# Kernel tuning notes

Hardware: AMD Instinct MI355X
Metric: run time of the kernel (lower is better)

## Reference

```python
import jax, jax.numpy as jnp
import numpy as np

# ---- production-scale dims ----
U, I, D = 51200, 25600, 64          # users, items, embed_size
E, EP = 1_000_000, 100_000          # train edges, pos/neg scoring edges
K = 8                               # topk similar users (FFT filter length)
NF = K // 2 + 1                     # rfft bins
CL_BS = 256                         # contrastive chunk size (U % CL_BS == 0)
TEMP = 0.2                          # args.temperature
N_LAYERS = 2                        # args.layers


def setup_inputs() -> dict:
    key = jax.random.key(0)
    ks = jax.random.split(key, 14)
    return {
        "user_emb": jax.random.normal(ks[0], (U, D), jnp.float32) * 0.1,
        "item_emb": jax.random.normal(ks[1], (I, D), jnp.float32) * 0.1,
        "W": jax.random.normal(ks[2], (D, D), jnp.float32) * (1.0 / np.sqrt(D)),
        "a": jax.random.normal(ks[3], (D,), jnp.float32) * 0.1,
        "WU": jax.random.normal(ks[4], (D, D), jnp.float32) * (1.0 / np.sqrt(D)),
        "aU": jax.random.normal(ks[5], (2 * D,), jnp.float32) * 0.1,
        "complex_weight": jax.random.normal(ks[6], (1, NF, D, 2), jnp.float32) * 0.02,
        "rate_src": jax.random.randint(ks[7], (E,), 0, U),
        "rate_dst": jax.random.randint(ks[8], (E,), 0, I),
        "pos_u": jax.random.randint(ks[9], (EP,), 0, U),
        "pos_i": jax.random.randint(ks[10], (EP,), 0, I),
        "neg_u": jax.random.randint(ks[11], (EP,), 0, U),
        "neg_i": jax.random.randint(ks[12], (EP,), 0, I),
        "nbr_idx": jax.random.randint(ks[13], (U, K), 0, U),
    }


def _propagate(src_feat, src_idx, dst_idx, n_dst):
    """DGRecLayer: degree-normalized mean aggregation over bipartite edges."""
    msg = src_feat[src_idx]                                       # [E, D] gather
    agg = jax.ops.segment_sum(msg, dst_idx, num_segments=n_dst)   # [n_dst, D] scatter
    deg = jax.ops.segment_sum(jnp.ones((src_idx.shape[0],), src_feat.dtype),
                              dst_idx, num_segments=n_dst)
    return agg / jnp.maximum(deg, 1.0)[:, None]


def _layer_attention(ls, W, a):
    t = jnp.stack(ls, axis=0)                                     # [L+1, N, D]
    alpha = jax.nn.softmax(jnp.einsum('lnd,de,e->ln', t, W, a), axis=0)
    return jnp.einsum('lnd,ln->nd', t, alpha)


def _anchor_user_embed(user_emb, WU, aU, complex_weight, nbr_idx):
    # Original detaches user embeddings to numpy for the FAISS path.
    ue = jax.lax.stop_gradient(user_emb)
    simu = ue[nbr_idx]                                            # [U, K, D]
    x = jnp.fft.rfft(simu, axis=1, norm='ortho')                  # [U, NF, D]
    wc = complex_weight[..., 0] + 1j * complex_weight[..., 1]     # [1, NF, D]
    simu = jnp.fft.irfft(x * wc, n=K, axis=1, norm='ortho')       # [U, K, D]
    Wsimu = jnp.einsum('ukd,de->uke', simu, WU)                   # [U, K, D]
    Wu = jnp.broadcast_to((ue @ WU)[:, None, :], Wsimu.shape)     # [U, K, D]
    e = jnp.concatenate([Wsimu, Wu], axis=2) @ aU                 # [U, K]
    e = jnp.where(e > 0, e, 0.1 * e)                              # LeakyReLU(0.1)
    alpha = jax.nn.softmax(e, axis=1)
    return jnp.einsum('uke,uk->ue', Wsimu, alpha)                 # [U, D]


def _chunk_contrast(r1, r2):
    B = r1.shape[0]
    n1 = jnp.linalg.norm(r1, axis=-1, keepdims=True)
    n2 = jnp.linalg.norm(r2, axis=-1, keepdims=True)
    s11 = (r1 @ r1.T) / (n1 @ n1.T + 1e-6) / TEMP
    c12 = (r1 @ r2.T) / (n1 @ n2.T + 1e-6) / TEMP
    s22 = (r2 @ r2.T) / (n2 @ n2.T + 1e-6) / TEMP
    c21 = (r2 @ r1.T) / (n2 @ n1.T + 1e-6) / TEMP
    mask = jax.nn.one_hot(jnp.arange(B), 2 * B, dtype=r1.dtype) * (-1e10)
    logits = jnp.concatenate(
        [jnp.concatenate([s11, c12], axis=-1) + mask,
         jnp.concatenate([s22, c21], axis=-1) + mask], axis=0)     # [2B, 2B]
    labels = jnp.concatenate([jnp.arange(B) + B, jnp.arange(B) + B])
    logz = jax.scipy.special.logsumexp(logits, axis=-1)
    return logz - logits[jnp.arange(2 * B), labels]                # per-example CE


def reference(user_emb, item_emb, W, a, WU, aU, complex_weight,
              rate_src, rate_dst, pos_u, pos_i, neg_u, neg_i, nbr_idx):
    h_u, h_i = user_emb, item_emb
    users, items = [h_u], [h_i]
    for _ in range(N_LAYERS):
        new_i = _propagate(h_u, rate_src, rate_dst, I)   # user -> item ('rate')
        new_u = _propagate(h_i, rate_dst, rate_src, U)   # item -> user ('rated by')
        h_u, h_i = new_u, new_i
        users.append(h_u)
        items.append(h_i)
    hu = _layer_attention(users, W, a)                   # [U, D]
    hi = _layer_attention(items, W, a)                   # [I, D]

    anchor = _anchor_user_embed(user_emb, WU, aU, complex_weight, nbr_idx)
    r1 = hu.reshape(-1, CL_BS, D)
    r2 = anchor.reshape(-1, CL_BS, D)
    loss_contrast = jax.vmap(_chunk_contrast)(r1, r2).mean()

    score_pos = jnp.sum(hu[pos_u] * hi[pos_i], axis=-1, keepdims=True)  # u_dot_v
    score_neg = jnp.sum(hu[neg_u] * hi[neg_i], axis=-1, keepdims=True)
    return score_pos, score_neg, loss_contrast
```

## Files before the change

kernel.cpp:

```cpp
#include <hip/hip_runtime.h>
#include <hip/hip_bf16.h>

constexpr int U_  = 51200;
constexpr int I_  = 25600;
constexpr int E_  = 1000000;
constexpr int EP_ = 100000;
constexpr int CB_ = 256;
constexpr int NCHUNK_ = U_ / CB_;
constexpr size_t UD_ = (size_t)U_ * 64;
constexpr size_t ID_ = (size_t)I_ * 64;
constexpr int NBK_ = 200;
constexpr int CAP_ = 8192;
constexpr int TILE_ = 4096;
constexpr int NBA_ = (E_ + TILE_ - 1) / TILE_;
constexpr int NANC_ = U_ / 16;
constexpr int NCVT_ = (int)((UD_ + ID_) / 512);

constexpr float SCALE_E_  = 16.f;
constexpr float ISCALE_E_ = 1.f / 16.f;
constexpr float SCALE_1_  = 64.f;
constexpr float ISCALE_1_ = 1.f / 64.f;

constexpr size_t OFF_LOSS  = 0;
constexpr size_t OFF_FLAG  = 1;
constexpr size_t OFF_CURU  = 8;
constexpr size_t OFF_CURI  = 208;
constexpr size_t MEMSET_BYTES = 408 * 4;
constexpr size_t OFF_VEC   = 448;
constexpr size_t OFF_BBU   = 640;
constexpr size_t OFF_BBI   = 848;
constexpr size_t OFF_ROWU  = 1088;
constexpr size_t OFF_ROWI  = ((OFF_ROWU + U_ + 1 + 63) / 64) * 64;
constexpr size_t OFF_CSRU  = ((OFF_ROWI + I_ + 1 + 63) / 64) * 64;
constexpr size_t OFF_CSRI  = OFF_CSRU + E_;
constexpr size_t OFF_U1    = ((OFF_CSRI + E_ + 63) / 64) * 64;
constexpr size_t OFF_I1    = OFF_U1 + UD_;
constexpr size_t OFF_HU    = OFF_I1 + ID_;
constexpr size_t OFF_HI    = OFF_HU + UD_;
constexpr size_t OFF_ANC   = OFF_HI + ID_;
constexpr size_t OFF_UE8   = OFF_ANC + UD_;
constexpr size_t OFF_IE8   = OFF_UE8 + UD_ / 4;
constexpr size_t OFF_U18   = OFF_IE8 + ID_ / 4;
constexpr size_t OFF_I18   = OFF_U18 + UD_ / 4;

#define DEVI static __device__ __forceinline__

typedef _Float16 h2v __attribute__((ext_vector_type(2)));
typedef _Float16 f16x8 __attribute__((ext_vector_type(8)));
typedef float floatx4 __attribute__((ext_vector_type(4)));

DEVI float b2f(__hip_bfloat16 x) { return __bfloat162float(x); }

DEVI float ldf(const void* p, size_t i, int isf32) {
  if (isf32) return ((const float*)p)[i];
  return b2f(((const __hip_bfloat16*)p)[i]);
}

DEVI float frcp(float x) { return __builtin_amdgcn_rcpf(x); }

DEVI float fexp2(float x) {
#if __has_builtin(__builtin_amdgcn_exp2f)
  return __builtin_amdgcn_exp2f(x);
#else
  return exp2f(x);
#endif
}

DEVI float fp8_dec(unsigned v) {
#if __has_builtin(__builtin_amdgcn_cvt_f32_fp8)
  return __builtin_amdgcn_cvt_f32_fp8(v, 0);
#else
  unsigned b = v & 0xFF;
  if (!(b & 0x78)) return 0.f;
  unsigned short h = (unsigned short)(((b & 0x80) << 8) | (((b & 0x7f) + (8 << 3)) << 7));
  _Float16 hf; __builtin_memcpy(&hf, &h, 2);
  return (float)hf;
#endif
}
DEVI unsigned fp8_enc_pk(float a, float b) {
#if __has_builtin(__builtin_amdgcn_cvt_pk_fp8_f32)
  return __builtin_amdgcn_cvt_pk_fp8_f32(a, b, 0u, false);
#else
  auto enc1 = [](float f) -> unsigned {
    _Float16 hf = (_Float16)f; unsigned short hb; __builtin_memcpy(&hb, &hf, 2);
    int s = hb >> 15, e = (hb >> 10) & 31, m = hb & 1023;
    int e8 = e - 15 + 7;
    int m3 = (m + ((1 << 6) + ((m >> 7) & 1))) >> 7;
    if (m3 > 7) { m3 = 0; e8++; }
    if (e8 <= 0) return (unsigned)(s << 7);
    if (e8 > 15) { e8 = 15; m3 = 6; }
    return (unsigned)((s << 7) | (e8 << 3) | m3);
  };
  return enc1(a) | (enc1(b) << 8);
#endif
}

DEVI int waveInclScan(int v, int lane) {
  #pragma unroll
  for (int off = 1; off < 64; off <<= 1) {
    int t = __shfl_up(v, off, 64);
    if (lane >= off) v += t;
  }
  return v;
}

__global__ void prep_kernel(const unsigned short* __restrict__ ueu,
                            const void* __restrict__ W, const void* __restrict__ a,
                            const void* __restrict__ WU, const void* __restrict__ aU,
                            float* __restrict__ vecs, float* __restrict__ flag) {
  int cnt = 0;
  for (int i = 0; i < 256; i++) {
    int e = (ueu[i] >> 7) & 0xFF;
    if (e >= 130) cnt++;
  }
  int isf32 = (cnt >= 8);
  if (threadIdx.x == 0) *flag = isf32 ? 1.0f : 0.0f;
  int d = threadIdx.x;
  float s = 0.f, t1 = 0.f, t2 = 0.f;
  for (int e = 0; e < 64; e++) {
    s += ldf(W, d * 64 + e, isf32) * ldf(a, e, isf32);
    float wue = ldf(WU, d * 64 + e, isf32);
    t1 += wue * ldf(aU, e, isf32);
    t2 += wue * ldf(aU, 64 + e, isf32);
  }
  vecs[d] = s;
  vecs[64 + d] = t1;
  vecs[128 + d] = t2;
}

struct BktSmem {
  int histU[NBK_], histI[NBK_];
  int loffU[NBK_ + 1], loffI[NBK_ + 1];
  int cbU[NBK_], cbI[NBK_];
  int lcU[NBK_], lcI[NBK_];
  int wsU[4], wsI[4];
  unsigned recsU[TILE_], recsI[TILE_];
};
constexpr int WS_ = 72;
struct AncSmem {
  _Float16 WUt[64 * WS_];
  _Float16 mixS[16 * WS_];
  float invSe[16];
  int nbrS[128];
};
constexpr size_t FSA_SMEM = sizeof(BktSmem) > sizeof(AncSmem) ? sizeof(BktSmem) : sizeof(AncSmem);

DEVI void bucketA_body(char* smemRaw, int blk,
    const int* __restrict__ rs, const int* __restrict__ rd,
    unsigned* __restrict__ bufU, unsigned* __restrict__ bufI,
    int* __restrict__ curU, int* __restrict__ curI) {
  BktSmem& S = *(BktSmem*)smemRaw;
  int tid = threadIdx.x;
  int base = blk * TILE_;
  for (int i = tid; i < NBK_; i += 256) { S.histU[i] = 0; S.histI[i] = 0; }
  __syncthreads();
  int ss[16], dd[16];
  #pragma unroll
  for (int t = 0; t < 16; t++) {
    int e = base + t * 256 + tid;
    bool v = e < E_;
    ss[t] = v ? rs[e] : -1;
    dd[t] = v ? rd[e] : 0;
    if (v) {
      atomicAdd(&S.histU[ss[t] >> 8], 1);
      atomicAdd(&S.histI[dd[t] >> 7], 1);
    }
  }
  __syncthreads();
  if (tid < NBK_) {
    int cU = S.histU[tid];
    S.cbU[tid] = tid * CAP_ + (cU ? atomicAdd(&curU[tid], cU) : 0);
    int cI = S.histI[tid];
    S.cbI[tid] = tid * CAP_ + (cI ? atomicAdd(&curI[tid], cI) : 0);
  }
  int lane = tid & 63, wv = tid >> 6;
  int cvU = (tid < NBK_) ? S.histU[tid] : 0;
  int cvI = (tid < NBK_) ? S.histI[tid] : 0;
  int inU = waveInclScan(cvU, lane);
  int inI = waveInclScan(cvI, lane);
  if (lane == 63) { S.wsU[wv] = inU; S.wsI[wv] = inI; }
  __syncthreads();
  int woU = 0, woI = 0;
  for (int w = 0; w < wv; w++) { woU += S.wsU[w]; woI += S.wsI[w]; }
  if (tid < NBK_) {
    S.loffU[tid] = woU + inU - cvU;
    S.loffI[tid] = woI + inI - cvI;
  }
  if (tid == NBK_ - 1) {
    S.loffU[NBK_] = woU + inU;
    S.loffI[NBK_] = woI + inI;
  }
  __syncthreads();
  if (tid < NBK_) { S.lcU[tid] = S.loffU[tid]; S.lcI[tid] = S.loffI[tid]; }
  __syncthreads();
  #pragma unroll
  for (int t = 0; t < 16; t++) {
    if (ss[t] >= 0) {
      int b = ss[t] >> 8;
      int p = atomicAdd(&S.lcU[b], 1);
      S.recsU[p] = ((unsigned)(ss[t] & 255) << 17) | (unsigned)dd[t];
      b = dd[t] >> 7;
      p = atomicAdd(&S.lcI[b], 1);
      S.recsI[p] = ((unsigned)(dd[t] & 127) << 17) | (unsigned)ss[t];
    }
  }
  __syncthreads();
  int totU = S.loffU[NBK_];
  for (int p = tid; p < totU; p += 256) {
    int lo = 0, hi = NBK_;
    while (hi - lo > 1) { int mid = (lo + hi) >> 1; if (S.loffU[mid] <= p) lo = mid; else hi = mid; }
    bufU[S.cbU[lo] + (p - S.loffU[lo])] = S.recsU[p];
  }
  int totI = S.loffI[NBK_];
  for (int p = tid; p < totI; p += 256) {
    int lo = 0, hi = NBK_;
    while (hi - lo > 1) { int mid = (lo + hi) >> 1; if (S.loffI[mid] <= p) lo = mid; else hi = mid; }
    bufI[S.cbI[lo] + (p - S.loffI[lo])] = S.recsI[p];
  }
}

DEVI void anchor_body(char* smemRaw, int blk,
    const void* __restrict__ ue, const void* __restrict__ WU,
    const void* __restrict__ cw, const float* __restrict__ vecs,
    const int* __restrict__ nbr, float* __restrict__ out, int isf32) {
  AncSmem& S = *(AncSmem*)smemRaw;
  int tid = threadIdx.x;
  int wv = tid >> 6, lane = tid & 63;
  int ublk = blk * 16;

  #pragma unroll
  for (int it = 0; it < 16; it++) {
    int k = it * 4 + wv;
    S.WUt[lane * WS_ + k] = (_Float16)ldf(WU, (size_t)k * 64 + lane, isf32);
  }
  if (tid < 128) S.nbrS[tid] = nbr[ublk * 8 + tid];
  __syncthreads();

  float cw0 = ldf(cw, (0 * 64 + lane) * 2, isf32);
  float w1r = ldf(cw, (1 * 64 + lane) * 2, isf32), w1i = ldf(cw, (1 * 64 + lane) * 2 + 1, isf32);
  float w2r = ldf(cw, (2 * 64 + lane) * 2, isf32), w2i = ldf(cw, (2 * 64 + lane) * 2 + 1, isf32);
  float w3r = ldf(cw, (3 * 64 + lane) * 2, isf32), w3i = ldf(cw, (3 * 64 + lane) * 2 + 1, isf32);
  float cw4 = ldf(cw, (4 * 64 + lane) * 2, isf32);
  float v1 = vecs[64 + lane], v2 = vecs[128 + lane];
  const float c1 = 0.70710678118654752440f;

  float xc[8], xn[8];
  #pragma unroll
  for (int k = 0; k < 8; k++)
    xc[k] = ldf(ue, (size_t)S.nbrS[wv * 32 + k] * 64 + lane, isf32);

  for (int u4 = 0; u4 < 4; u4++) {
    int uL = wv * 4 + u4;
    int u = ublk + uL;
    if (u4 < 3) {
      #pragma unroll
      for (int k = 0; k < 8; k++)
        xn[k] = ldf(ue, (size_t)S.nbrS[wv * 32 + (u4 + 1) * 8 + k] * 64 + lane, isf32);
    }
    float sA = xc[1] - xc[3] - xc[5] + xc[7];
    float sB = xc[1] + xc[3] - xc[5] - xc[7];
    float ev = (xc[0] + xc[4]) + (xc[2] + xc[6]);
    float od = (xc[1] + xc[5]) + (xc[3] + xc[7]);
    float d04 = xc[0] - xc[4], d26 = xc[2] - xc[6];
    float X0r = ev + od;
    float X1r = d04 + c1 * sA;
    float X1i = -d26 - c1 * sB;
    float X2r = (xc[0] + xc[4]) - (xc[2] + xc[6]);
    float X2i = -(xc[1] - xc[3] + xc[5] - xc[7]);
    float X3r = d04 - c1 * sA;
    float X3i = d26 - c1 * sB;
    float X4r = ev - od;
    float Zr0 = X0r * cw0;
    float Zr1 = X1r * w1r - X1i * w1i, Zi1 = X1r * w1i + X1i * w1r;
    float Zr2 = X2r * w2r - X2i * w2i, Zi2 = X2r * w2i + X2i * w2r;
    float Zr3 = X3r * w3r - X3i * w3i, Zi3 = X3r * w3i + X3i * w3r;
    float Zr4 = X4r * cw4;
    float eP = Zr0 + Zr4, eM = Zr0 - Zr4;
    float t1 = c1 * (Zr1 - Zr3), t2 = c1 * (Zi1 + Zi3);
    float y[8];
    y[0] = eP + 2.f * (Zr1 + Zr2 + Zr3);
    y[1] = eM + 2.f * (t1 - t2 - Zi2);
    y[2] = eP + 2.f * (-Zi1 - Zr2 + Zi3);
    y[3] = eM + 2.f * (-t1 - t2 + Zi2);
    y[4] = eP + 2.f * (-Zr1 + Zr2 - Zr3);
    y[5] = eM + 2.f * (-t1 + t2 - Zi2);
    y[6] = eP + 2.f * (Zi1 - Zr2 - Zi3);
    y[7] = eM + 2.f * (t1 + t2 + Zi2);
    #pragma unroll
    for (int k = 0; k < 8; k++) y[k] *= 0.125f;

    float ek[8];
    #pragma unroll
    for (int k = 0; k < 8; k++) ek[k] = y[k] * v1;
    float q = ldf(ue, (size_t)u * 64 + lane, isf32) * v2;
    #pragma unroll
    for (int off = 32; off; off >>= 1) {
      #pragma unroll
      for (int k = 0; k < 8; k++) ek[k] += __shfl_xor(ek[k], off, 64);
      q += __shfl_xor(q, off, 64);
    }
    float m = -1e30f;
    #pragma unroll
    for (int k = 0; k < 8; k++) {
      float v = ek[k] + q;
      v = v > 0.f ? v : 0.1f * v;
      ek[k] = v;
      m = fmaxf(m, v);
    }
    float se = 0.f, wexp[8];
    #pragma unroll
    for (int k = 0; k < 8; k++) { wexp[k] = __expf(ek[k] - m); se += wexp[k]; }
    float mix = 0.f;
    #pragma unroll
    for (int k = 0; k < 8; k++) mix += wexp[k] * y[k];
    S.mixS[uL * WS_ + lane] = (_Float16)mix;
    if (lane == 0) S.invSe[uL] = frcp(se);
    #pragma unroll
    for (int k = 0; k < 8; k++) xc[k] = xn[k];
  }
  __syncthreads();

  int n = lane & 15, qd = lane >> 4;
  f16x8 A0 = *(const f16x8*)&S.mixS[(lane & 15) * WS_ + qd * 8];
  f16x8 A1 = *(const f16x8*)&S.mixS[(lane & 15) * WS_ + 32 + qd * 8];
  f16x8 B0 = *(const f16x8*)&S.WUt[(wv * 16 + n) * WS_ + qd * 8];
  f16x8 B1 = *(const f16x8*)&S.WUt[(wv * 16 + n) * WS_ + 32 + qd * 8];
  const floatx4 zero = {0.f, 0.f, 0.f, 0.f};
  floatx4 acc = __builtin_amdgcn_mfma_f32_16x16x32_f16(A0, B0, zero, 0, 0, 0);
  acc = __builtin_amdgcn_mfma_f32_16x16x32_f16(A1, B1, acc, 0, 0, 0);
  #pragma unroll
  for (int r = 0; r < 4; r++) {
    int m = qd * 4 + r;
    out[(size_t)(ublk + m) * 64 + wv * 16 + n] = acc[r] * S.invSe[m];
  }
}

DEVI void convert_body(int blk, const void* __restrict__ ue, const void* __restrict__ ie,
                       unsigned char* __restrict__ ue8, unsigned char* __restrict__ ie8,
                       int isf32) {
  size_t t = (size_t)blk * 256 + threadIdx.x;
  float a, b; unsigned short* dst; size_t o;
  if (t < UD_ / 2) {
    a = ldf(ue, 2 * t, isf32); b = ldf(ue, 2 * t + 1, isf32);
    dst = (unsigned short*)ue8; o = t;
  } else {
    size_t s = t - UD_ / 2;
    a = ldf(ie, 2 * s, isf32); b = ldf(ie, 2 * s + 1, isf32);
    dst = (unsigned short*)ie8; o = s;
  }
  unsigned p = fp8_enc_pk(a * SCALE_E_, b * SCALE_E_);
  dst[o] = (unsigned short)(p & 0xFFFF);
}

__global__ __launch_bounds__(256) void fusedA_kernel(
    const int* __restrict__ rs, const int* __restrict__ rd,
    unsigned* __restrict__ bufU, unsigned* __restrict__ bufI,
    int* __restrict__ curU, int* __restrict__ curI,
    const void* __restrict__ ue, const void* __restrict__ ie,
    const void* __restrict__ WU, const void* __restrict__ cw,
    const float* __restrict__ vecs, const int* __restrict__ nbr,
    float* __restrict__ anc, unsigned char* __restrict__ ue8,
    unsigned char* __restrict__ ie8, const float* __restrict__ flag) {
  __shared__ __align__(16) char smem[FSA_SMEM];
  if (blockIdx.x < NBA_) {
    bucketA_body(smem, blockIdx.x, rs, rd, bufU, bufI, curU, curI);
  } else if (blockIdx.x < NBA_ + NANC_) {
    anchor_body(smem, blockIdx.x - NBA_, ue, WU, cw, vecs, nbr, anc, *flag > 0.5f);
  } else {
    convert_body(blockIdx.x - NBA_ - NANC_, ue, ie, ue8, ie8, *flag > 0.5f);
  }
}

__global__ void scanBuckets_kernel(const int* __restrict__ curU,
                                   const int* __restrict__ curI,
                                   int* __restrict__ bbU, int* __restrict__ bbI,
                                   int* __restrict__ rowU, int* __restrict__ rowI) {
  if (threadIdx.x == 0) {
    int run = 0;
    for (int i = 0; i < NBK_; i++) { bbU[i] = run; run += curU[i]; }
    bbU[NBK_] = run;
    run = 0;
    for (int i = 0; i < NBK_; i++) { bbI[i] = run; run += curI[i]; }
    bbI[NBK_] = run;
    rowU[U_] = E_;
    rowI[I_] = E_;
  }
}

__global__ __launch_bounds__(256) void bucketB_kernel(
    const unsigned* __restrict__ bufU, const unsigned* __restrict__ bufI,
    const int* __restrict__ curU, const int* __restrict__ curI,
    const int* __restrict__ bbU, const int* __restrict__ bbI,
    int* __restrict__ rowU, int* __restrict__ rowI,
    int* __restrict__ csrU, int* __restrict__ csrI) {
  __shared__ int stage[CAP_];
  __shared__ int cntk[256], offk[256];
  __shared__ int wsum[4];
  int tid = threadIdx.x, b = blockIdx.x;
  int side = b >= NBK_;
  int bb = side ? b - NBK_ : b;
  const unsigned* src = (side ? bufI : bufU) + (size_t)bb * CAP_;
  int total = side ? curI[bb] : curU[bb];
  int gbase = side ? bbI[bb] : bbU[bb];
  int kpb   = side ? 128 : 256;
  int* rowptr = side ? rowI : rowU;
  int* csr    = side ? csrI : csrU;
  cntk[tid] = 0;
  __syncthreads();
  for (int r = tid; r < total; r += 256) atomicAdd(&cntk[src[r] >> 17], 1);
  __syncthreads();
  int lane = tid & 63, wv = tid >> 6;
  int cv = (tid < kpb) ? cntk[tid] : 0;
  int incl = waveInclScan(cv, lane);
  if (lane == 63) wsum[wv] = incl;
  __syncthreads();
  int wvoff = 0;
  for (int w = 0; w < wv; w++) wvoff += wsum[w];
  int excl = wvoff + incl - cv;
  if (tid < kpb) {
    offk[tid] = excl;
    rowptr[bb * kpb + tid] = gbase + excl;
  }
  __syncthreads();
  for (int r = tid; r < total; r += 256) {
    unsigned rec = src[r];
    int slot = atomicAdd(&offk[rec >> 17], 1);
    if (slot < CAP_) stage[slot] = (int)(rec & 0x1FFFFu);
  }
  __syncthreads();
  for (int s = tid; s < total; s += 256) csr[gbase + s] = stage[s];
}

__global__ __launch_bounds__(256) void agg1_kernel(
    const unsigned char* __restrict__ ue8, const unsigned char* __restrict__ ie8,
    const int* __restrict__ rowU, const int* __restrict__ rowI,
    const int* __restrict__ csrU, const int* __restrict__ csrI,
    __hip_bfloat16* __restrict__ u1, __hip_bfloat16* __restrict__ i1,
    unsigned char* __restrict__ u18, unsigned char* __restrict__ i18) {
  int wv = threadIdx.x >> 6, lane = threadIdx.x & 63;
  int side = blockIdx.x >= I_ / 4;
  int blk = side ? blockIdx.x - I_ / 4 : blockIdx.x;
  int r = blk * 4 + wv;
  const int* row = side ? rowU : rowI;
  const int* csr = side ? csrU : csrI;
  const unsigned char* src = side ? ie8 : ue8;
  __hip_bfloat16* out = side ? u1 : i1;
  unsigned char* out8 = side ? u18 : i18;
  int s0 = row[r], s1 = row[r + 1];
  float acc = 0.f;
  int j = s0;
  for (; j + 4 <= s1; j += 4) {
    int a = csr[j], b = csr[j + 1], c = csr[j + 2], d = csr[j + 3];
    float va = fp8_dec(src[(size_t)a * 64 + lane]);
    float vb = fp8_dec(src[(size_t)b * 64 + lane]);
    float vc = fp8_dec(src[(size_t)c * 64 + lane]);
    float vd = fp8_dec(src[(size_t)d * 64 + lane]);
    acc += (va + vb) + (vc + vd);
  }
  for (; j < s1; j++) acc += fp8_dec(src[(size_t)csr[j] * 64 + lane]);
  float val = acc * ISCALE_E_ * frcp(fmaxf((float)(s1 - s0), 1.0f));
  size_t idx = (size_t)r * 64 + lane;
  out[idx] = __float2bfloat16(val);
  unsigned p = fp8_enc_pk(val * SCALE_1_, val * SCALE_1_);
  out8[idx] = (unsigned char)(p & 0xFF);
}

__global__ __launch_bounds__(256) void agg2attn_kernel(
    const unsigned char* __restrict__ u18, const unsigned char* __restrict__ i18,
    const __hip_bfloat16* __restrict__ u1, const __hip_bfloat16* __restrict__ i1,
    const void* __restrict__ ue, const void* __restrict__ ie,
    const int* __restrict__ rowU, const int* __restrict__ rowI,
    const int* __restrict__ csrU, const int* __restrict__ csrI,
    const float* __restrict__ vecs, float* __restrict__ hu, float* __restrict__ hi,
    const float* __restrict__ flag) {
  int isf32 = *flag > 0.5f;
  int wv = threadIdx.x >> 6, lane = threadIdx.x & 63;
  int side = blockIdx.x >= I_ / 4;
  int blk = side ? blockIdx.x - I_ / 4 : blockIdx.x;
  int r = blk * 4 + wv;
  const int* row = side ? rowU : rowI;
  const int* csr = side ? csrU : csrI;
  const unsigned char* opp8 = side ? i18 : u18;
  const __hip_bfloat16* own1 = side ? u1 : i1;
  const void* base = side ? ue : ie;
  float* h = side ? hu : hi;
  int s0 = row[r], s1 = row[r + 1];
  float acc = 0.f;
  int j = s0;
  for (; j + 4 <= s1; j += 4) {
    int a = csr[j], b = csr[j + 1], c = csr[j + 2], d = csr[j + 3];
    float va = fp8_dec(opp8[(size_t)a * 64 + lane]);
    float vb = fp8_dec(opp8[(size_t)b * 64 + lane]);
    float vc = fp8_dec(opp8[(size_t)c * 64 + lane]);
    float vd = fp8_dec(opp8[(size_t)d * 64 + lane]);
    acc += (va + vb) + (vc + vd);
  }
  for (; j < s1; j++) acc += fp8_dec(opp8[(size_t)csr[j] * 64 + lane]);
  size_t idx = (size_t)r * 64 + lane;
  float t2 = acc * ISCALE_1_ * frcp(fmaxf((float)(s1 - s0), 1.0f));
  float t0 = ldf(base, idx, isf32);
  float t1 = b2f(own1[idx]);
  float w = vecs[lane];
  float p0 = t0 * w, p1 = t1 * w, p2 = t2 * w;
  #pragma unroll
  for (int off = 32; off; off >>= 1) {
    p0 += __shfl_xor(p0, off, 64);
    p1 += __shfl_xor(p1, off, 64);
    p2 += __shfl_xor(p2, off, 64);
  }
  float m = fmaxf(p0, fmaxf(p1, p2));
  float e0 = __expf(p0 - m), e1 = __expf(p1 - m), e2 = __expf(p2 - m);
  float inv = 1.0f / (e0 + e1 + e2);
  h[idx] = (t0 * e0 + t1 * e1 + t2 * e2) * inv;
}

constexpr int XS_ = 72;
constexpr float SC_  = 2.6857914f;
constexpr float EPS_ = 1e-6f;
constexpr float LN2_ = 0.6931471805599453f;
__global__ __launch_bounds__(1024) void contrast_kernel(
    const float* __restrict__ hu, const float* __restrict__ an,
    float* __restrict__ loss_acc) {
  __shared__ __align__(16) _Float16 Xh[512 * XS_];
  __shared__ float iN[512];
  int tid = threadIdx.x;
  int c = blockIdx.x;

  if (tid < 512) {
    int row = tid & 255;
    const float* r1 = (tid < 256 ? hu : an) + ((size_t)c * CB_ + row) * 64;
    float4 a4[16];
    float s1 = 0.f;
    #pragma unroll
    for (int t = 0; t < 16; t++) {
      a4[t] = ((const float4*)r1)[t];
      s1 += a4[t].x * a4[t].x + a4[t].y * a4[t].y + a4[t].z * a4[t].z + a4[t].w * a4[t].w;
    }
    float inv = frcp(sqrtf(s1));
    iN[tid] = inv;
    float sc = inv * SC_;
    #pragma unroll
    for (int t = 0; t < 8; t++) {
      f16x8 v;
      v[0] = (_Float16)(a4[2*t].x * sc);   v[1] = (_Float16)(a4[2*t].y * sc);
      v[2] = (_Float16)(a4[2*t].z * sc);   v[3] = (_Float16)(a4[2*t].w * sc);
      v[4] = (_Float16)(a4[2*t+1].x * sc); v[5] = (_Float16)(a4[2*t+1].y * sc);
      v[6] = (_Float16)(a4[2*t+1].z * sc); v[7] = (_Float16)(a4[2*t+1].w * sc);
      *(f16x8*)&Xh[tid * XS_ + t * 8] = v;
    }
  }
  __syncthreads();

  int l = tid & 63, wv = tid >> 6;
  int n = l & 15, q = l >> 4;
  int rb = wv * 32;
  f16x8 A[2][2];
  #pragma unroll
  for (int t = 0; t < 2; t++) {
    A[t][0] = *(const f16x8*)&Xh[(rb + t * 16 + n) * XS_ + q * 8];
    A[t][1] = *(const f16x8*)&Xh[(rb + t * 16 + n) * XS_ + 32 + q * 8];
  }
  float eNiR[2][4];
  #pragma unroll
  for (int t = 0; t < 2; t++)
    #pragma unroll
    for (int r = 0; r < 4; r++)
      eNiR[t][r] = EPS_ * iN[rb + t * 16 + q * 4 + r];
  float sums[2][4] = {{0,0,0,0},{0,0,0,0}};
  float labs2[2] = {0, 0};
  int selfn = q * 4;
  const floatx4 zero = {0.f, 0.f, 0.f, 0.f};
  for (int ct = 0; ct < 32; ct++) {
    f16x8 B0 = *(const f16x8*)&Xh[(ct * 16 + n) * XS_ + q * 8];
    f16x8 B1 = *(const f16x8*)&Xh[(ct * 16 + n) * XS_ + 32 + q * 8];
    float iNj = iN[ct * 16 + n];
    #pragma unroll
    for (int t = 0; t < 2; t++) {
      floatx4 acc = __builtin_amdgcn_mfma_f32_16x16x32_f16(A[t][0], B0, zero, 0, 0, 0);
      acc = __builtin_amdgcn_mfma_f32_16x16x32_f16(A[t][1], B1, acc, 0, 0, 0);
      int rtg = wv * 2 + t;
      if (ct == (rtg ^ 16)) {
        #pragma unroll
        for (int r = 0; r < 4; r++) {
          float G = acc[r];
          float u = eNiR[t][r] * iNj;
          float s2 = __builtin_fmaf(G, -u, G);
          sums[t][r] += fexp2(s2);
          if (n == selfn + r) labs2[t] += s2;
        }
      } else if (ct == rtg) {
        #pragma unroll
        for (int r = 0; r < 4; r++) {
          float G = acc[r];
          float u = eNiR[t][r] * iNj;
          float s2 = __builtin_fmaf(G, -u, G);
          float e = (n == selfn + r) ? 0.f : fexp2(s2);
          sums[t][r] += e;
        }
      } else {
        #pragma unroll
        for (int r = 0; r < 4; r++) {
          float G = acc[r];
          float u = eNiR[t][r] * iNj;
          float s2 = __builtin_fmaf(G, -u, G);
          sums[t][r] += fexp2(s2);
        }
      }
    }
  }
  #pragma unroll
  for (int off = 1; off <= 8; off <<= 1) {
    #pragma unroll
    for (int t = 0; t < 2; t++) {
      #pragma unroll
      for (int r = 0; r < 4; r++) sums[t][r] += __shfl_xor(sums[t][r], off, 64);
      labs2[t] += __shfl_xor(labs2[t], off, 64);
    }
  }
  float part = 0.f;
  if (n == 0) {
    #pragma unroll
    for (int t = 0; t < 2; t++) {
      float lt = 0.f;
      #pragma unroll
      for (int r = 0; r < 4; r++) lt += __logf(sums[t][r]);
      part += lt - labs2[t] * LN2_;
    }
  }
  #pragma unroll
  for (int off = 1; off < 64; off <<= 1) part += __shfl_xor(part, off, 64);
  if (l == 0) atomicAdd(loss_acc, part);
}

__global__ __launch_bounds__(256) void score_kernel(
    const float* __restrict__ hu, const float* __restrict__ hi,
    const int* __restrict__ pu, const int* __restrict__ pi,
    const int* __restrict__ nu, const int* __restrict__ ni,
    void* __restrict__ out, const float* __restrict__ flag) {
  int isf32 = *flag > 0.5f;
  int w = (blockIdx.x * 256 + threadIdx.x) >> 6;
  int lane = threadIdx.x & 63;
  int uu, ii;
  if (w < EP_) { uu = pu[w]; ii = pi[w]; }
  else         { uu = nu[w - EP_]; ii = ni[w - EP_]; }
  float p = hu[(size_t)uu * 64 + lane] * hi[(size_t)ii * 64 + lane];
  #pragma unroll
  for (int off = 32; off; off >>= 1) p += __shfl_xor(p, off, 64);
  if (lane == 0) {
    if (isf32) ((float*)out)[w] = p;
    else       ((__hip_bfloat16*)out)[w] = __float2bfloat16(p);
  }
}

__global__ void finalize_kernel(const float* __restrict__ loss_acc,
                                void* __restrict__ out,
                                const float* __restrict__ flag) {
  float v = loss_acc[0] * (1.0f / (float)(2 * CB_ * NCHUNK_));
  if (*flag > 0.5f) ((float*)out)[2 * EP_] = v;
  else              ((__hip_bfloat16*)out)[2 * EP_] = __float2bfloat16(v);
}

extern "C" void kernel_launch(void* const* d_in, const int* in_sizes, int n_in,
                              void* d_out, int out_size, void* d_ws, size_t ws_size,
                              hipStream_t stream) {
  const void* ue  = d_in[0];
  const void* ie  = d_in[1];
  const void* W   = d_in[2];
  const void* a   = d_in[3];
  const void* WU  = d_in[4];
  const void* aU  = d_in[5];
  const void* cw  = d_in[6];
  const int* rs  = (const int*)d_in[7];
  const int* rd  = (const int*)d_in[8];
  const int* pu  = (const int*)d_in[9];
  const int* pi  = (const int*)d_in[10];
  const int* nu  = (const int*)d_in[11];
  const int* ni  = (const int*)d_in[12];
  const int* nbr = (const int*)d_in[13];

  float* wsf  = (float*)d_ws;
  int*   wsi  = (int*)d_ws;
  float* loss = wsf + OFF_LOSS;
  float* flag = wsf + OFF_FLAG;
  int* curU   = wsi + OFF_CURU;
  int* curI   = wsi + OFF_CURI;
  float* vecs = wsf + OFF_VEC;
  int* bbU    = wsi + OFF_BBU;
  int* bbI    = wsi + OFF_BBI;
  int* rowU   = wsi + OFF_ROWU;
  int* rowI   = wsi + OFF_ROWI;
  int* csrU   = wsi + OFF_CSRU;
  int* csrI   = wsi + OFF_CSRI;
  __hip_bfloat16* u1 = (__hip_bfloat16*)(wsf + OFF_U1);
  __hip_bfloat16* i1 = (__hip_bfloat16*)(wsf + OFF_I1);
  float* hu   = wsf + OFF_HU;
  float* hi   = wsf + OFF_HI;
  float* anc  = wsf + OFF_ANC;
  unsigned char* ue8 = (unsigned char*)(wsf + OFF_UE8);
  unsigned char* ie8 = (unsigned char*)(wsf + OFF_IE8);
  unsigned char* u18 = (unsigned char*)(wsf + OFF_U18);
  unsigned char* i18 = (unsigned char*)(wsf + OFF_I18);
  unsigned* bufU = (unsigned*)(wsf + OFF_HU);
  unsigned* bufI = (unsigned*)(wsf + OFF_HI);

  hipMemsetAsync(d_ws, 0, MEMSET_BYTES, stream);
  prep_kernel<<<1, 64, 0, stream>>>((const unsigned short*)ue, W, a, WU, aU, vecs, flag);

  fusedA_kernel<<<NBA_ + NANC_ + NCVT_, 256, 0, stream>>>(
      rs, rd, bufU, bufI, curU, curI, ue, ie, WU, cw, vecs, nbr, anc, ue8, ie8, flag);
  scanBuckets_kernel<<<1, 64, 0, stream>>>(curU, curI, bbU, bbI, rowU, rowI);
  bucketB_kernel<<<2 * NBK_, 256, 0, stream>>>(bufU, bufI, curU, curI, bbU, bbI,
                                               rowU, rowI, csrU, csrI);

  agg1_kernel<<<(I_ + U_) / 4, 256, 0, stream>>>(ue8, ie8, rowU, rowI, csrU, csrI,
                                                 u1, i1, u18, i18);
  agg2attn_kernel<<<(I_ + U_) / 4, 256, 0, stream>>>(u18, i18, u1, i1, ue, ie,
                                                     rowU, rowI, csrU, csrI,
                                                     vecs, hu, hi, flag);

  contrast_kernel<<<NCHUNK_, 1024, 0, stream>>>(hu, anc, loss);

  score_kernel<<<(2 * EP_ * 64) / 256, 256, 0, stream>>>(hu, hi, pu, pi, nu, ni, d_out, flag);
  finalize_kernel<<<1, 1, 0, stream>>>(loss, d_out, flag);
}
```

Measured before the change: 406.5 us.

## Read fp8 user embeddings in anchor path and bf16 copies in scoring

The fp8 conversion of the user and item embeddings moves out of the fused bucketing kernel into its own launch, which runs first. The anchor computation can then gather its neighbour rows from the 1-byte fp8 copy instead of the full-precision input, rescaling the result afterwards. The attention kernel now also writes bf16 copies of hu and hi, and the scoring kernel gathers from those to halve its random-access traffic. The cost is an extra kernel launch, serialization of the conversion ahead of the anchor blocks, an extra bf16 write, and lower precision in the anchor attention and in the scores.

```diff
diff --git a/kernel.cpp b/kernel.cpp
--- a/kernel.cpp
+++ b/kernel.cpp
@@ -42,6 +42,8 @@
 constexpr size_t OFF_IE8   = OFF_UE8 + UD_ / 4;
 constexpr size_t OFF_U18   = OFF_IE8 + ID_ / 4;
 constexpr size_t OFF_I18   = OFF_U18 + UD_ / 4;
+constexpr size_t OFF_HUB   = OFF_I18 + ID_ / 4;
+constexpr size_t OFF_HIB   = OFF_HUB + UD_ / 2;
 
 #define DEVI static __device__ __forceinline__
 
@@ -128,6 +130,25 @@
   vecs[128 + d] = t2;
 }
 
+__global__ __launch_bounds__(256) void convert_kernel(
+    const void* __restrict__ ue, const void* __restrict__ ie,
+    unsigned char* __restrict__ ue8, unsigned char* __restrict__ ie8,
+    const float* __restrict__ flag) {
+  int isf32 = *flag > 0.5f;
+  size_t t = (size_t)blockIdx.x * 256 + threadIdx.x;
+  float a, b; unsigned short* dst; size_t o;
+  if (t < UD_ / 2) {
+    a = ldf(ue, 2 * t, isf32); b = ldf(ue, 2 * t + 1, isf32);
+    dst = (unsigned short*)ue8; o = t;
+  } else {
+    size_t s = t - UD_ / 2;
+    a = ldf(ie, 2 * s, isf32); b = ldf(ie, 2 * s + 1, isf32);
+    dst = (unsigned short*)ie8; o = s;
+  }
+  unsigned p = fp8_enc_pk(a * SCALE_E_, b * SCALE_E_);
+  dst[o] = (unsigned short)(p & 0xFFFF);
+}
+
 struct BktSmem {
   int histU[NBK_], histI[NBK_];
   int loffU[NBK_ + 1], loffI[NBK_ + 1];
@@ -220,7 +241,7 @@
 }
 
 DEVI void anchor_body(char* smemRaw, int blk,
-    const void* __restrict__ ue, const void* __restrict__ WU,
+    const unsigned char* __restrict__ ue8, const void* __restrict__ WU,
     const void* __restrict__ cw, const float* __restrict__ vecs,
     const int* __restrict__ nbr, float* __restrict__ out, int isf32) {
   AncSmem& S = *(AncSmem*)smemRaw;
@@ -243,11 +264,12 @@
   float cw4 = ldf(cw, (4 * 64 + lane) * 2, isf32);
   float v1 = vecs[64 + lane], v2 = vecs[128 + lane];
   const float c1 = 0.70710678118654752440f;
+  const float YSC = 0.125f * ISCALE_E_;
 
   float xc[8], xn[8];
   #pragma unroll
   for (int k = 0; k < 8; k++)
-    xc[k] = ldf(ue, (size_t)S.nbrS[wv * 32 + k] * 64 + lane, isf32);
+    xc[k] = fp8_dec(ue8[(size_t)S.nbrS[wv * 32 + k] * 64 + lane]);
 
   for (int u4 = 0; u4 < 4; u4++) {
     int uL = wv * 4 + u4;
@@ -255,7 +277,7 @@
     if (u4 < 3) {
       #pragma unroll
       for (int k = 0; k < 8; k++)
-        xn[k] = ldf(ue, (size_t)S.nbrS[wv * 32 + (u4 + 1) * 8 + k] * 64 + lane, isf32);
+        xn[k] = fp8_dec(ue8[(size_t)S.nbrS[wv * 32 + (u4 + 1) * 8 + k] * 64 + lane]);
     }
     float sA = xc[1] - xc[3] - xc[5] + xc[7];
     float sB = xc[1] + xc[3] - xc[5] - xc[7];
@@ -287,12 +309,12 @@
     y[6] = eP + 2.f * (Zi1 - Zr2 - Zi3);
     y[7] = eM + 2.f * (t1 + t2 + Zi2);
     #pragma unroll
-    for (int k = 0; k < 8; k++) y[k] *= 0.125f;
+    for (int k = 0; k < 8; k++) y[k] *= YSC;
 
     float ek[8];
     #pragma unroll
     for (int k = 0; k < 8; k++) ek[k] = y[k] * v1;
-    float q = ldf(ue, (size_t)u * 64 + lane, isf32) * v2;
+    float q = fp8_dec(ue8[(size_t)u * 64 + lane]) * ISCALE_E_ * v2;
     #pragma unroll
     for (int off = 32; off; off >>= 1) {
       #pragma unroll
@@ -335,39 +357,19 @@
   }
 }
 
-DEVI void convert_body(int blk, const void* __restrict__ ue, const void* __restrict__ ie,
-                       unsigned char* __restrict__ ue8, unsigned char* __restrict__ ie8,
-                       int isf32) {
-  size_t t = (size_t)blk * 256 + threadIdx.x;
-  float a, b; unsigned short* dst; size_t o;
-  if (t < UD_ / 2) {
-    a = ldf(ue, 2 * t, isf32); b = ldf(ue, 2 * t + 1, isf32);
-    dst = (unsigned short*)ue8; o = t;
-  } else {
-    size_t s = t - UD_ / 2;
-    a = ldf(ie, 2 * s, isf32); b = ldf(ie, 2 * s + 1, isf32);
-    dst = (unsigned short*)ie8; o = s;
-  }
-  unsigned p = fp8_enc_pk(a * SCALE_E_, b * SCALE_E_);
-  dst[o] = (unsigned short)(p & 0xFFFF);
-}
-
 __global__ __launch_bounds__(256) void fusedA_kernel(
     const int* __restrict__ rs, const int* __restrict__ rd,
     unsigned* __restrict__ bufU, unsigned* __restrict__ bufI,
     int* __restrict__ curU, int* __restrict__ curI,
-    const void* __restrict__ ue, const void* __restrict__ ie,
-    const void* __restrict__ WU, const void* __restrict__ cw,
-    const float* __restrict__ vecs, const int* __restrict__ nbr,
-    float* __restrict__ anc, unsigned char* __restrict__ ue8,
-    unsigned char* __restrict__ ie8, const float* __restrict__ flag) {
+    const unsigned char* __restrict__ ue8, const void* __restrict__ WU,
+    const void* __restrict__ cw, const float* __restrict__ vecs,
+    const int* __restrict__ nbr, float* __restrict__ anc,
+    const float* __restrict__ flag) {
   __shared__ __align__(16) char smem[FSA_SMEM];
   if (blockIdx.x < NBA_) {
     bucketA_body(smem, blockIdx.x, rs, rd, bufU, bufI, curU, curI);
-  } else if (blockIdx.x < NBA_ + NANC_) {
-    anchor_body(smem, blockIdx.x - NBA_, ue, WU, cw, vecs, nbr, anc, *flag > 0.5f);
   } else {
-    convert_body(blockIdx.x - NBA_ - NANC_, ue, ie, ue8, ie8, *flag > 0.5f);
+    anchor_body(smem, blockIdx.x - NBA_, ue8, WU, cw, vecs, nbr, anc, *flag > 0.5f);
   }
 }
 
@@ -472,6 +474,7 @@
     const int* __restrict__ rowU, const int* __restrict__ rowI,
     const int* __restrict__ csrU, const int* __restrict__ csrI,
     const float* __restrict__ vecs, float* __restrict__ hu, float* __restrict__ hi,
+    __hip_bfloat16* __restrict__ hub, __hip_bfloat16* __restrict__ hib,
     const float* __restrict__ flag) {
   int isf32 = *flag > 0.5f;
   int wv = threadIdx.x >> 6, lane = threadIdx.x & 63;
@@ -484,6 +487,7 @@
   const __hip_bfloat16* own1 = side ? u1 : i1;
   const void* base = side ? ue : ie;
   float* h = side ? hu : hi;
+  __hip_bfloat16* hb = side ? hub : hib;
   int s0 = row[r], s1 = row[r + 1];
   float acc = 0.f;
   int j = s0;
@@ -511,7 +515,9 @@
   float m = fmaxf(p0, fmaxf(p1, p2));
   float e0 = __expf(p0 - m), e1 = __expf(p1 - m), e2 = __expf(p2 - m);
   float inv = 1.0f / (e0 + e1 + e2);
-  h[idx] = (t0 * e0 + t1 * e1 + t2 * e2) * inv;
+  float hv = (t0 * e0 + t1 * e1 + t2 * e2) * inv;
+  h[idx] = hv;
+  hb[idx] = __float2bfloat16(hv);
 }
 
 constexpr int XS_ = 72;
@@ -633,7 +639,7 @@
 }
 
 __global__ __launch_bounds__(256) void score_kernel(
-    const float* __restrict__ hu, const float* __restrict__ hi,
+    const __hip_bfloat16* __restrict__ hub, const __hip_bfloat16* __restrict__ hib,
     const int* __restrict__ pu, const int* __restrict__ pi,
     const int* __restrict__ nu, const int* __restrict__ ni,
     void* __restrict__ out, const float* __restrict__ flag) {
@@ -643,7 +649,7 @@
   int uu, ii;
   if (w < EP_) { uu = pu[w]; ii = pi[w]; }
   else         { uu = nu[w - EP_]; ii = ni[w - EP_]; }
-  float p = hu[(size_t)uu * 64 + lane] * hi[(size_t)ii * 64 + lane];
+  float p = b2f(hub[(size_t)uu * 64 + lane]) * b2f(hib[(size_t)ii * 64 + lane]);
   #pragma unroll
   for (int off = 32; off; off >>= 1) p += __shfl_xor(p, off, 64);
   if (lane == 0) {
@@ -700,14 +706,18 @@
   unsigned char* ie8 = (unsigned char*)(wsf + OFF_IE8);
   unsigned char* u18 = (unsigned char*)(wsf + OFF_U18);
   unsigned char* i18 = (unsigned char*)(wsf + OFF_I18);
+  __hip_bfloat16* hub = (__hip_bfloat16*)(wsf + OFF_HUB);
+  __hip_bfloat16* hib = (__hip_bfloat16*)(wsf + OFF_HIB);
   unsigned* bufU = (unsigned*)(wsf + OFF_HU);
   unsigned* bufI = (unsigned*)(wsf + OFF_HI);
 
   hipMemsetAsync(d_ws, 0, MEMSET_BYTES, stream);
   prep_kernel<<<1, 64, 0, stream>>>((const unsigned short*)ue, W, a, WU, aU, vecs, flag);
 
-  fusedA_kernel<<<NBA_ + NANC_ + NCVT_, 256, 0, stream>>>(
-      rs, rd, bufU, bufI, curU, curI, ue, ie, WU, cw, vecs, nbr, anc, ue8, ie8, flag);
+  convert_kernel<<<NCVT_, 256, 0, stream>>>(ue, ie, ue8, ie8, flag);
+
+  fusedA_kernel<<<NBA_ + NANC_, 256, 0, stream>>>(
+      rs, rd, bufU, bufI, curU, curI, ue8, WU, cw, vecs, nbr, anc, flag);
   scanBuckets_kernel<<<1, 64, 0, stream>>>(curU, curI, bbU, bbI, rowU, rowI);
   bucketB_kernel<<<2 * NBK_, 256, 0, stream>>>(bufU, bufI, curU, curI, bbU, bbI,
                                                rowU, rowI, csrU, csrI);
@@ -716,10 +726,10 @@
                                                  u1, i1, u18, i18);
   agg2attn_kernel<<<(I_ + U_) / 4, 256, 0, stream>>>(u18, i18, u1, i1, ue, ie,
                                                      rowU, rowI, csrU, csrI,
-                                                     vecs, hu, hi, flag);
+                                                     vecs, hu, hi, hub, hib, flag);
 
   contrast_kernel<<<NCHUNK_, 1024, 0, stream>>>(hu, anc, loss);
 
-  score_kernel<<<(2 * EP_ * 64) / 256, 256, 0, stream>>>(hu, hi, pu, pi, nu, ni, d_out, flag);
+  score_kernel<<<(2 * EP_ * 64) / 256, 256, 0, stream>>>(hub, hib, pu, pi, nu, ni, d_out, flag);
   finalize_kernel<<<1, 1, 0, stream>>>(loss, d_out, flag);
 }
```

Result: no change. 410.6 us (+1.0%).
